# Performance work log

Measured on AMD Instinct MI355X. Metric: run time of the kernel, lower is better.

Reference implementation:

```python
import jax, jax.numpy as jnp
import numpy as np

P = 7          # output_size
SCALE = 0.125  # spatial_scale
S = 2          # sampling_ratio


def setup_inputs() -> dict:
    key = jax.random.key(0)
    k1, k2, k3, k4, k5, k6 = jax.random.split(key, 6)
    N, C, H, W, R = 8, 256, 100, 100, 512
    x = jax.random.normal(k1, (N, C, H, W), dtype=jnp.float32)
    b = jax.random.randint(k2, (R,), 0, N).astype(jnp.float32)
    x1 = jax.random.uniform(k3, (R,)) * 600.0
    y1 = jax.random.uniform(k4, (R,)) * 600.0
    bw = 10.0 + jax.random.uniform(k5, (R,)) * 190.0
    bh = 10.0 + jax.random.uniform(k6, (R,)) * 190.0
    rois = jnp.stack([b, x1, y1, x1 + bw, y1 + bh], axis=1).astype(jnp.float32)
    return {"x": x, "rois": rois}


def _axis_terms(c, L):
    # Per-axis bilinear terms, matching torchvision bilinear_interpolate.
    valid = (c > -1.0) & (c < L)          # whole sample zeroed if out of range
    c = jnp.clip(c, 0.0, L - 1.0)          # low clamp at 0; >=L-1 -> frac 0
    lo = jnp.minimum(jnp.floor(c).astype(jnp.int32), L - 1)
    hi = jnp.minimum(lo + 1, L - 1)
    frac = c - lo.astype(c.dtype)
    w_lo = jnp.where(valid, 1.0 - frac, 0.0)
    w_hi = jnp.where(valid, frac, 0.0)
    return lo, hi, w_lo, w_hi


def roi_align(x, rois):
    # aligned=True RoIAlign. x: [N,C,H,W], rois: [R,5] -> [R,C,P,P]
    N, C, H, W = x.shape
    b = rois[:, 0].astype(jnp.int32)
    sx = rois[:, 1] * SCALE - 0.5
    sy = rois[:, 2] * SCALE - 0.5
    bin_w = (rois[:, 3] * SCALE - 0.5 - sx) / P
    bin_h = (rois[:, 4] * SCALE - 0.5 - sy) / P

    frac = (jnp.arange(S, dtype=x.dtype) + 0.5) / S   # sample offset within bin
    bins = jnp.arange(P, dtype=x.dtype)
    grid = bins[None, :, None] + frac[None, None, :]   # [1,P,S]
    ys = sy[:, None, None] + grid * bin_h[:, None, None]  # [R,P,S]
    xs = sx[:, None, None] + grid * bin_w[:, None, None]  # [R,P,S]

    yl, yh, wy1, wy2 = _axis_terms(ys, H)
    xl, xh, wx1, wx2 = _axis_terms(xs, W)

    bb = b[:, None, None, None, None]
    Yl, Yh = yl[:, :, :, None, None], yh[:, :, :, None, None]  # [R,P,S,1,1]
    Xl, Xh = xl[:, None, None, :, :], xh[:, None, None, :, :]  # [R,1,1,P,S]

    def g(Y, X):
        # gather -> [R,Py,Sy,Px,Sx,C]
        return x[bb, :, Y, X]

    def w(wy, wx):
        return (wy[:, :, :, None, None] * wx[:, None, None, :, :])[..., None]

    val = (g(Yl, Xl) * w(wy1, wx1) + g(Yl, Xh) * w(wy1, wx2)
           + g(Yh, Xl) * w(wy2, wx1) + g(Yh, Xh) * w(wy2, wx2))
    # average over the SxS sampling grid per bin
    out = val.sum(axis=(2, 4)) / float(S * S)   # [R,Py,Px,C]
    return jnp.transpose(out, (0, 3, 1, 2))      # [R,C,P,P]


def reference(x, rois):
    return roi_align(x, rois)
```

## Files before the change

kernel.cpp:

```cpp
#include <hip/hip_runtime.h>

#define POOL 7
#define CCH 256
#define HH 100
#define WW 100
#define HW (HH * WW)
#define MAXTH 28
#define NTAP 14
#define NT 256
#define ITEMS 2
#define SLOTF 896

static constexpr float SCALE = 0.125f;

__device__ __forceinline__ void tap_calc(float s0, float step, int k, int L,
                                         int& lo, int& hi, float& w1, float& w2)
{
    const int   p  = k >> 1, si = k & 1;
    const float g  = (float)p + ((float)si + 0.5f) * 0.5f;
    const float c  = s0 + g * step;
    const float Lf = (float)L;
    const bool  valid = (c > -1.0f) && (c < Lf);
    float cl = fminf(fmaxf(c, 0.0f), Lf - 1.0f);
    lo = (int)floorf(cl);
    if (lo > L - 1) lo = L - 1;
    hi = lo + 1;
    if (hi > L - 1) hi = L - 1;
    const float fr = cl - (float)lo;
    w1 = valid ? 1.0f - fr : 0.0f;
    w2 = valid ? fr : 0.0f;
}

__device__ __forceinline__ void tap_x(float s0, float step, int k,
                                      int& lo, float& w1, float& w2)
{
    int hi;
    tap_calc(s0, step, k, WW, lo, hi, w1, w2);
    if (hi == lo) { w1 += w2; w2 = 0.0f; }
}

template <int NJ>
__device__ __forceinline__ void run2(
    const float* __restrict__ x, float* __restrict__ out,
    float* slot, int n, int c0, int r, int xmin_al, int ymin,
    int TWp, int tot, int magic, int nb4, int lane,
    int xlo0, float wx10, float wx20, int xlo1, float wx11, float wx21,
    const int4& yt0, const int4& yt1, int bin)
{
    const float* xa = x + ((size_t)(n * CCH + c0)) * HW
                        + (size_t)ymin * WW + xmin_al;
    const float* xb = xa + HW;

    #pragma unroll
    for (int j = 0; j < NJ; ++j) {
        const int idx = lane + 64 * j;
        const int row = (idx * magic) >> 16;
        const int b   = idx - row * nb4;
        const int go  = row * WW + (b << 2);
        float* la = slot + j * 256;
        float* lb = slot + SLOTF + j * 256;
        if (j < NJ - 1 || idx < tot) {
            __builtin_amdgcn_global_load_lds(
                (const __attribute__((address_space(1))) void*)(xa + go),
                (__attribute__((address_space(3))) void*)la, 16, 0, 0);
            __builtin_amdgcn_global_load_lds(
                (const __attribute__((address_space(1))) void*)(xb + go),
                (__attribute__((address_space(3))) void*)lb, 16, 0, 0);
        }
    }

    int   off[8];
    float wgt[16];
    {
        const int   rl0 = yt0.x * TWp, rh0 = yt0.y * TWp;
        const int   rl1 = yt1.x * TWp, rh1 = yt1.y * TWp;
        const float wy10 = __int_as_float(yt0.z), wy20 = __int_as_float(yt0.w);
        const float wy11 = __int_as_float(yt1.z), wy21 = __int_as_float(yt1.w);
        off[0] = rl0 + xlo0;  wgt[0]  = wy10 * wx10;  wgt[1]  = wy10 * wx20;
        off[1] = rl0 + xlo1;  wgt[2]  = wy10 * wx11;  wgt[3]  = wy10 * wx21;
        off[2] = rh0 + xlo0;  wgt[4]  = wy20 * wx10;  wgt[5]  = wy20 * wx20;
        off[3] = rh0 + xlo1;  wgt[6]  = wy20 * wx11;  wgt[7]  = wy20 * wx21;
        off[4] = rl1 + xlo0;  wgt[8]  = wy11 * wx10;  wgt[9]  = wy11 * wx20;
        off[5] = rl1 + xlo1;  wgt[10] = wy11 * wx11;  wgt[11] = wy11 * wx21;
        off[6] = rh1 + xlo0;  wgt[12] = wy21 * wx10;  wgt[13] = wy21 * wx20;
        off[7] = rh1 + xlo1;  wgt[14] = wy21 * wx11;  wgt[15] = wy21 * wx21;
    }

    asm volatile("s_waitcnt vmcnt(1)" ::: "memory");
    float a0 = 0.f, a1 = 0.f, a2 = 0.f, a3 = 0.f;
    #pragma unroll
    for (int p = 0; p < 8; p += 4) {
        a0 += wgt[2*p + 0] * slot[off[p + 0]] + wgt[2*p + 1] * slot[off[p + 0] + 1];
        a1 += wgt[2*p + 2] * slot[off[p + 1]] + wgt[2*p + 3] * slot[off[p + 1] + 1];
        a2 += wgt[2*p + 4] * slot[off[p + 2]] + wgt[2*p + 5] * slot[off[p + 2] + 1];
        a3 += wgt[2*p + 6] * slot[off[p + 3]] + wgt[2*p + 7] * slot[off[p + 3] + 1];
    }
    const float accA = (a0 + a1) + (a2 + a3);

    asm volatile("s_waitcnt vmcnt(0)" ::: "memory");
    const float* sb = slot + SLOTF;
    float b0 = 0.f, b1 = 0.f, b2 = 0.f, b3 = 0.f;
    #pragma unroll
    for (int p = 0; p < 8; p += 4) {
        b0 += wgt[2*p + 0] * sb[off[p + 0]] + wgt[2*p + 1] * sb[off[p + 0] + 1];
        b1 += wgt[2*p + 2] * sb[off[p + 1]] + wgt[2*p + 3] * sb[off[p + 1] + 1];
        b2 += wgt[2*p + 4] * sb[off[p + 2]] + wgt[2*p + 5] * sb[off[p + 2] + 1];
        b3 += wgt[2*p + 6] * sb[off[p + 3]] + wgt[2*p + 7] * sb[off[p + 3] + 1];
    }
    const float accB = (b0 + b1) + (b2 + b3);

    if (lane < POOL * POOL) {
        float* ob = out + ((size_t)(r * CCH + c0)) * (POOL * POOL) + bin;
        ob[0]           = accA * 0.25f;
        ob[POOL * POOL] = accB * 0.25f;
    }
}

__global__ __launch_bounds__(NT) void roi_main(
    const float* __restrict__ x, const float* __restrict__ rois,
    float* __restrict__ out)
{
    __shared__ float tile[(NT / 64) * ITEMS * SLOTF];

    const int bid  = blockIdx.x;
    const int r    = bid >> 5;
    const int g    = bid & 31;
    const int wid  = threadIdx.x >> 6;
    const int lane = threadIdx.x & 63;
    const int c0   = g * (ITEMS * NT / 64) + wid * ITEMS;

    const float r0  = rois[r * 5 + 0];
    const float sx0 = rois[r * 5 + 1] * SCALE - 0.5f;
    const float sy0 = rois[r * 5 + 2] * SCALE - 0.5f;
    const float bw  = (rois[r * 5 + 3] * SCALE - 0.5f - sx0) * (1.0f / POOL);
    const float bh  = (rois[r * 5 + 4] * SCALE - 0.5f - sy0) * (1.0f / POOL);
    const int   n   = (int)r0;

    int xl0, xh0, xl13, xh13, yl0d, yh0d, yl13, yh13; float ua, ub;
    tap_calc(sx0, bw, 0,        WW, xl0,  xh0,  ua, ub);
    tap_calc(sx0, bw, NTAP - 1, WW, xl13, xh13, ua, ub);
    tap_calc(sy0, bh, 0,        HH, yl0d, yh0d, ua, ub);
    tap_calc(sy0, bh, NTAP - 1, HH, yl13, yh13, ua, ub);
    const int xmin_al = xl0 & ~3;
    const int ymin    = yl0d;
    int TH  = yh13 - ymin + 1; if (TH > MAXTH) TH = MAXTH;
    int nb4 = ((xh13 - xmin_al) >> 2) + 1;  if (nb4 > 8) nb4 = 8;
    const int magic = (int)ceilf(65536.0f / (float)nb4);
    const int tot   = TH * nb4;
    const int TWp   = nb4 << 2;
    const int nj    = (tot + 63) >> 6;

    const int bin = (lane < POOL * POOL) ? lane : POOL * POOL - 1;
    const int py  = bin / POOL;
    const int px  = bin - py * POOL;

    int xlo0, xlo1; float wx10, wx20, wx11, wx21;
    {
        int lo; float w1, w2;
        tap_x(sx0, bw, px * 2,     lo, w1, w2);
        xlo0 = max(lo - xmin_al, 0); wx10 = w1; wx20 = w2;
        tap_x(sx0, bw, px * 2 + 1, lo, w1, w2);
        xlo1 = max(lo - xmin_al, 0); wx11 = w1; wx21 = w2;
    }
    int4 yt0, yt1;
    {
        int lo, hi; float w1, w2;
        tap_calc(sy0, bh, py * 2,     HH, lo, hi, w1, w2);
        yt0 = make_int4(max(lo - ymin, 0), max(hi - ymin, 0),
                        __float_as_int(w1), __float_as_int(w2));
        tap_calc(sy0, bh, py * 2 + 1, HH, lo, hi, w1, w2);
        yt1 = make_int4(max(lo - ymin, 0), max(hi - ymin, 0),
                        __float_as_int(w1), __float_as_int(w2));
    }

    float* slot = tile + wid * (ITEMS * SLOTF);

    switch (nj) {
    case 1:  run2<1>(x, out, slot, n, c0, r, xmin_al, ymin, TWp, tot, magic, nb4, lane, xlo0, wx10, wx20, xlo1, wx11, wx21, yt0, yt1, bin); break;
    case 2:  run2<2>(x, out, slot, n, c0, r, xmin_al, ymin, TWp, tot, magic, nb4, lane, xlo0, wx10, wx20, xlo1, wx11, wx21, yt0, yt1, bin); break;
    case 3:  run2<3>(x, out, slot, n, c0, r, xmin_al, ymin, TWp, tot, magic, nb4, lane, xlo0, wx10, wx20, xlo1, wx11, wx21, yt0, yt1, bin); break;
    default: run2<4>(x, out, slot, n, c0, r, xmin_al, ymin, TWp, tot, magic, nb4, lane, xlo0, wx10, wx20, xlo1, wx11, wx21, yt0, yt1, bin); break;
    }
}

extern "C" void kernel_launch(void* const* d_in, const int* in_sizes, int n_in,
                              void* d_out, int out_size, void* d_ws, size_t ws_size,
                              hipStream_t stream) {
    const float* x    = (const float*)d_in[0];
    const float* rois = (const float*)d_in[1];
    float*       out  = (float*)d_out;

    const int R = in_sizes[1] / 5;
    roi_main<<<R * 32, NT, 0, stream>>>(x, rois, out);
}
```

Baseline: 36.97 us.

## Process four channels per wave with double-buffered LDS async loads

Each wave now handles four channels instead of two. It reuses two LDS slots in a ping-pong pipeline: the loads for channel k+2 are issued once the compute on channel k has drained its LDS reads. The grid is halved to 16 blocks per ROI, and the bin/tile bounds come from per-lane tap results via readlane instead of extra tap_calc calls. The aim is to amortize per-block setup and overlap global-to-LDS loads with compute, at the cost of fewer blocks in flight and longer serial chains per wave.

```diff
diff --git a/kernel.cpp b/kernel.cpp
--- a/kernel.cpp
+++ b/kernel.cpp
@@ -8,7 +8,7 @@
 #define MAXTH 28
 #define NTAP 14
 #define NT 256
-#define ITEMS 2
+#define ITEMS 4
 #define SLOTF 896
 
 static constexpr float SCALE = 0.125f;
@@ -31,51 +31,148 @@
     w2 = valid ? fr : 0.0f;
 }
 
-__device__ __forceinline__ void tap_x(float s0, float step, int k,
-                                      int& lo, float& w1, float& w2)
-{
-    int hi;
-    tap_calc(s0, step, k, WW, lo, hi, w1, w2);
-    if (hi == lo) { w1 += w2; w2 = 0.0f; }
-}
-
 template <int NJ>
-__device__ __forceinline__ void run2(
+__device__ __forceinline__ void run4(
     const float* __restrict__ x, float* __restrict__ out,
     float* slot, int n, int c0, int r, int xmin_al, int ymin,
     int TWp, int tot, int magic, int nb4, int lane,
-    int xlo0, float wx10, float wx20, int xlo1, float wx11, float wx21,
-    const int4& yt0, const int4& yt1, int bin)
+    const int* off, const float* wgt, int bin)
 {
-    const float* xa = x + ((size_t)(n * CCH + c0)) * HW
-                        + (size_t)ymin * WW + xmin_al;
-    const float* xb = xa + HW;
-
+    const float* xc[ITEMS];
+    {
+        const float* xa = x + ((size_t)(n * CCH + c0)) * HW
+                            + (size_t)ymin * WW + xmin_al;
+        #pragma unroll
+        for (int k = 0; k < ITEMS; ++k) xc[k] = xa + (size_t)k * HW;
+    }
+    float* slotB = slot + SLOTF;
+
+    int go[NJ]; bool act[NJ];
     #pragma unroll
     for (int j = 0; j < NJ; ++j) {
         const int idx = lane + 64 * j;
         const int row = (idx * magic) >> 16;
         const int b   = idx - row * nb4;
-        const int go  = row * WW + (b << 2);
-        float* la = slot + j * 256;
-        float* lb = slot + SLOTF + j * 256;
-        if (j < NJ - 1 || idx < tot) {
-            __builtin_amdgcn_global_load_lds(
-                (const __attribute__((address_space(1))) void*)(xa + go),
-                (__attribute__((address_space(3))) void*)la, 16, 0, 0);
-            __builtin_amdgcn_global_load_lds(
-                (const __attribute__((address_space(1))) void*)(xb + go),
-                (__attribute__((address_space(3))) void*)lb, 16, 0, 0);
-        }
-    }
+        go[j]  = row * WW + (b << 2);
+        act[j] = (j < NJ - 1) || (idx < tot);
+    }
+
+#define ISSUE(k, dst)                                                        \
+    _Pragma("unroll")                                                        \
+    for (int j = 0; j < NJ; ++j)                                             \
+        if (act[j])                                                          \
+            __builtin_amdgcn_global_load_lds(                                \
+                (const __attribute__((address_space(1))) void*)(xc[k] + go[j]), \
+                (__attribute__((address_space(3))) void*)((dst) + j * 256),  \
+                16, 0, 0);
+
+#define COMPUTE(dst, buf)                                                    \
+    {                                                                        \
+        float a0 = 0.f, a1 = 0.f, a2 = 0.f, a3 = 0.f;                        \
+        _Pragma("unroll")                                                    \
+        for (int p = 0; p < 8; p += 4) {                                     \
+            a0 += wgt[2*p+0] * (buf)[off[p+0]] + wgt[2*p+1] * (buf)[off[p+0]+1]; \
+            a1 += wgt[2*p+2] * (buf)[off[p+1]] + wgt[2*p+3] * (buf)[off[p+1]+1]; \
+            a2 += wgt[2*p+4] * (buf)[off[p+2]] + wgt[2*p+5] * (buf)[off[p+2]+1]; \
+            a3 += wgt[2*p+6] * (buf)[off[p+3]] + wgt[2*p+7] * (buf)[off[p+3]+1]; \
+        }                                                                    \
+        dst = (a0 + a1) + (a2 + a3);                                         \
+    }
+
+    ISSUE(0, slot)
+    ISSUE(1, slotB)
+
+    float acc0, acc1, acc2, acc3;
+
+    asm volatile("s_waitcnt vmcnt(%0)" :: "n"(NJ) : "memory");
+    COMPUTE(acc0, slot)
+    asm volatile("s_waitcnt lgkmcnt(0)" ::: "memory");
+    __builtin_amdgcn_sched_barrier(0);
+    ISSUE(2, slot)
+
+    asm volatile("s_waitcnt vmcnt(%0)" :: "n"(NJ) : "memory");
+    COMPUTE(acc1, slotB)
+    asm volatile("s_waitcnt lgkmcnt(0)" ::: "memory");
+    __builtin_amdgcn_sched_barrier(0);
+    ISSUE(3, slotB)
+
+    asm volatile("s_waitcnt vmcnt(%0)" :: "n"(NJ) : "memory");
+    COMPUTE(acc2, slot)
+
+    asm volatile("s_waitcnt vmcnt(0)" ::: "memory");
+    COMPUTE(acc3, slotB)
+
+#undef ISSUE
+#undef COMPUTE
+
+    if (lane < POOL * POOL) {
+        float* ob = out + ((size_t)(r * CCH + c0)) * (POOL * POOL) + bin;
+        ob[0 * POOL * POOL] = acc0 * 0.25f;
+        ob[1 * POOL * POOL] = acc1 * 0.25f;
+        ob[2 * POOL * POOL] = acc2 * 0.25f;
+        ob[3 * POOL * POOL] = acc3 * 0.25f;
+    }
+}
+
+__global__ __launch_bounds__(NT) void roi_main(
+    const float* __restrict__ x, const float* __restrict__ rois,
+    float* __restrict__ out)
+{
+    __shared__ float tile[(NT / 64) * 2 * SLOTF];
+
+    const int bid  = blockIdx.x;
+    const int r    = bid >> 4;
+    const int g    = bid & 15;
+    const int wid  = threadIdx.x >> 6;
+    const int lane = threadIdx.x & 63;
+    const int c0   = g * (ITEMS * NT / 64) + wid * ITEMS;
+
+    const float r0  = rois[r * 5 + 0];
+    const float sx0 = rois[r * 5 + 1] * SCALE - 0.5f;
+    const float sy0 = rois[r * 5 + 2] * SCALE - 0.5f;
+    const float bw  = (rois[r * 5 + 3] * SCALE - 0.5f - sx0) * (1.0f / POOL);
+    const float bh  = (rois[r * 5 + 4] * SCALE - 0.5f - sy0) * (1.0f / POOL);
+    const int   n   = (int)r0;
+
+    const int bin = (lane < POOL * POOL) ? lane : POOL * POOL - 1;
+    const int py  = bin / POOL;
+    const int px  = bin - py * POOL;
+
+    int xlo0r, xlo1r; float wx10, wx20, wx11, wx21;
+    {
+        int lo, hi; float w1, w2;
+        tap_calc(sx0, bw, px * 2,     WW, lo, hi, w1, w2);
+        if (hi == lo) { w1 += w2; w2 = 0.0f; }
+        xlo0r = lo; wx10 = w1; wx20 = w2;
+        tap_calc(sx0, bw, px * 2 + 1, WW, lo, hi, w1, w2);
+        if (hi == lo) { w1 += w2; w2 = 0.0f; }
+        xlo1r = lo; wx11 = w1; wx21 = w2;
+    }
+    int ylo0r, yhi0r, ylo1r, yhi1r; float wy10, wy20, wy11, wy21;
+    tap_calc(sy0, bh, py * 2,     HH, ylo0r, yhi0r, wy10, wy20);
+    tap_calc(sy0, bh, py * 2 + 1, HH, ylo1r, yhi1r, wy11, wy21);
+
+    const int xmin_al = __builtin_amdgcn_readlane(xlo0r, 0) & ~3;
+    const int ymin    = __builtin_amdgcn_readlane(ylo0r, 0);
+    const int xmaxr   = __builtin_amdgcn_readlane(xlo1r, 48);
+    const int ymaxr   = __builtin_amdgcn_readlane(yhi1r, 48);
+    int TH  = ymaxr - ymin + 1;             if (TH > MAXTH) TH = MAXTH;
+    int nb4 = ((min(xmaxr + 1, WW - 1) - xmin_al) >> 2) + 1;
+    if (nb4 > 8) nb4 = 8;
+    const int magic = (int)ceilf(65536.0f / (float)nb4);
+    const int tot   = TH * nb4;
+    const int TWp   = nb4 << 2;
+    const int nj    = (tot + 63) >> 6;
 
     int   off[8];
     float wgt[16];
     {
-        const int   rl0 = yt0.x * TWp, rh0 = yt0.y * TWp;
-        const int   rl1 = yt1.x * TWp, rh1 = yt1.y * TWp;
-        const float wy10 = __int_as_float(yt0.z), wy20 = __int_as_float(yt0.w);
-        const float wy11 = __int_as_float(yt1.z), wy21 = __int_as_float(yt1.w);
+        const int xlo0 = max(xlo0r - xmin_al, 0);
+        const int xlo1 = max(xlo1r - xmin_al, 0);
+        const int rl0  = max(ylo0r - ymin, 0) * TWp;
+        const int rh0  = max(yhi0r - ymin, 0) * TWp;
+        const int rl1  = max(ylo1r - ymin, 0) * TWp;
+        const int rh1  = max(yhi1r - ymin, 0) * TWp;
         off[0] = rl0 + xlo0;  wgt[0]  = wy10 * wx10;  wgt[1]  = wy10 * wx20;
         off[1] = rl0 + xlo1;  wgt[2]  = wy10 * wx11;  wgt[3]  = wy10 * wx21;
         off[2] = rh0 + xlo0;  wgt[4]  = wy20 * wx10;  wgt[5]  = wy20 * wx20;
@@ -86,100 +183,13 @@
         off[7] = rh1 + xlo1;  wgt[14] = wy21 * wx11;  wgt[15] = wy21 * wx21;
     }
 
-    asm volatile("s_waitcnt vmcnt(1)" ::: "memory");
-    float a0 = 0.f, a1 = 0.f, a2 = 0.f, a3 = 0.f;
-    #pragma unroll
-    for (int p = 0; p < 8; p += 4) {
-        a0 += wgt[2*p + 0] * slot[off[p + 0]] + wgt[2*p + 1] * slot[off[p + 0] + 1];
-        a1 += wgt[2*p + 2] * slot[off[p + 1]] + wgt[2*p + 3] * slot[off[p + 1] + 1];
-        a2 += wgt[2*p + 4] * slot[off[p + 2]] + wgt[2*p + 5] * slot[off[p + 2] + 1];
-        a3 += wgt[2*p + 6] * slot[off[p + 3]] + wgt[2*p + 7] * slot[off[p + 3] + 1];
-    }
-    const float accA = (a0 + a1) + (a2 + a3);
-
-    asm volatile("s_waitcnt vmcnt(0)" ::: "memory");
-    const float* sb = slot + SLOTF;
-    float b0 = 0.f, b1 = 0.f, b2 = 0.f, b3 = 0.f;
-    #pragma unroll
-    for (int p = 0; p < 8; p += 4) {
-        b0 += wgt[2*p + 0] * sb[off[p + 0]] + wgt[2*p + 1] * sb[off[p + 0] + 1];
-        b1 += wgt[2*p + 2] * sb[off[p + 1]] + wgt[2*p + 3] * sb[off[p + 1] + 1];
-        b2 += wgt[2*p + 4] * sb[off[p + 2]] + wgt[2*p + 5] * sb[off[p + 2] + 1];
-        b3 += wgt[2*p + 6] * sb[off[p + 3]] + wgt[2*p + 7] * sb[off[p + 3] + 1];
-    }
-    const float accB = (b0 + b1) + (b2 + b3);
-
-    if (lane < POOL * POOL) {
-        float* ob = out + ((size_t)(r * CCH + c0)) * (POOL * POOL) + bin;
-        ob[0]           = accA * 0.25f;
-        ob[POOL * POOL] = accB * 0.25f;
-    }
-}
-
-__global__ __launch_bounds__(NT) void roi_main(
-    const float* __restrict__ x, const float* __restrict__ rois,
-    float* __restrict__ out)
-{
-    __shared__ float tile[(NT / 64) * ITEMS * SLOTF];
-
-    const int bid  = blockIdx.x;
-    const int r    = bid >> 5;
-    const int g    = bid & 31;
-    const int wid  = threadIdx.x >> 6;
-    const int lane = threadIdx.x & 63;
-    const int c0   = g * (ITEMS * NT / 64) + wid * ITEMS;
-
-    const float r0  = rois[r * 5 + 0];
-    const float sx0 = rois[r * 5 + 1] * SCALE - 0.5f;
-    const float sy0 = rois[r * 5 + 2] * SCALE - 0.5f;
-    const float bw  = (rois[r * 5 + 3] * SCALE - 0.5f - sx0) * (1.0f / POOL);
-    const float bh  = (rois[r * 5 + 4] * SCALE - 0.5f - sy0) * (1.0f / POOL);
-    const int   n   = (int)r0;
-
-    int xl0, xh0, xl13, xh13, yl0d, yh0d, yl13, yh13; float ua, ub;
-    tap_calc(sx0, bw, 0,        WW, xl0,  xh0,  ua, ub);
-    tap_calc(sx0, bw, NTAP - 1, WW, xl13, xh13, ua, ub);
-    tap_calc(sy0, bh, 0,        HH, yl0d, yh0d, ua, ub);
-    tap_calc(sy0, bh, NTAP - 1, HH, yl13, yh13, ua, ub);
-    const int xmin_al = xl0 & ~3;
-    const int ymin    = yl0d;
-    int TH  = yh13 - ymin + 1; if (TH > MAXTH) TH = MAXTH;
-    int nb4 = ((xh13 - xmin_al) >> 2) + 1;  if (nb4 > 8) nb4 = 8;
-    const int magic = (int)ceilf(65536.0f / (float)nb4);
-    const int tot   = TH * nb4;
-    const int TWp   = nb4 << 2;
-    const int nj    = (tot + 63) >> 6;
-
-    const int bin = (lane < POOL * POOL) ? lane : POOL * POOL - 1;
-    const int py  = bin / POOL;
-    const int px  = bin - py * POOL;
-
-    int xlo0, xlo1; float wx10, wx20, wx11, wx21;
-    {
-        int lo; float w1, w2;
-        tap_x(sx0, bw, px * 2,     lo, w1, w2);
-        xlo0 = max(lo - xmin_al, 0); wx10 = w1; wx20 = w2;
-        tap_x(sx0, bw, px * 2 + 1, lo, w1, w2);
-        xlo1 = max(lo - xmin_al, 0); wx11 = w1; wx21 = w2;
-    }
-    int4 yt0, yt1;
-    {
-        int lo, hi; float w1, w2;
-        tap_calc(sy0, bh, py * 2,     HH, lo, hi, w1, w2);
-        yt0 = make_int4(max(lo - ymin, 0), max(hi - ymin, 0),
-                        __float_as_int(w1), __float_as_int(w2));
-        tap_calc(sy0, bh, py * 2 + 1, HH, lo, hi, w1, w2);
-        yt1 = make_int4(max(lo - ymin, 0), max(hi - ymin, 0),
-                        __float_as_int(w1), __float_as_int(w2));
-    }
-
-    float* slot = tile + wid * (ITEMS * SLOTF);
+    float* slot = tile + wid * (2 * SLOTF);
 
     switch (nj) {
-    case 1:  run2<1>(x, out, slot, n, c0, r, xmin_al, ymin, TWp, tot, magic, nb4, lane, xlo0, wx10, wx20, xlo1, wx11, wx21, yt0, yt1, bin); break;
-    case 2:  run2<2>(x, out, slot, n, c0, r, xmin_al, ymin, TWp, tot, magic, nb4, lane, xlo0, wx10, wx20, xlo1, wx11, wx21, yt0, yt1, bin); break;
-    case 3:  run2<3>(x, out, slot, n, c0, r, xmin_al, ymin, TWp, tot, magic, nb4, lane, xlo0, wx10, wx20, xlo1, wx11, wx21, yt0, yt1, bin); break;
-    default: run2<4>(x, out, slot, n, c0, r, xmin_al, ymin, TWp, tot, magic, nb4, lane, xlo0, wx10, wx20, xlo1, wx11, wx21, yt0, yt1, bin); break;
+    case 1:  run4<1>(x, out, slot, n, c0, r, xmin_al, ymin, TWp, tot, magic, nb4, lane, off, wgt, bin); break;
+    case 2:  run4<2>(x, out, slot, n, c0, r, xmin_al, ymin, TWp, tot, magic, nb4, lane, off, wgt, bin); break;
+    case 3:  run4<3>(x, out, slot, n, c0, r, xmin_al, ymin, TWp, tot, magic, nb4, lane, off, wgt, bin); break;
+    default: run4<4>(x, out, slot, n, c0, r, xmin_al, ymin, TWp, tot, magic, nb4, lane, off, wgt, bin); break;
     }
 }
 
@@ -191,5 +201,5 @@
     float*       out  = (float*)d_out;
 
     const int R = in_sizes[1] / 5;
-    roi_main<<<R * 32, NT, 0, stream>>>(x, rois, out);
-}
+    roi_main<<<R * 16, NT, 0, stream>>>(x, rois, out);
+}
```

New measurement: 34.84 us, median of 2. 1.06x faster.
